# Optimization experiments

Hardware: AMD Instinct MI355X
Metric: run time of the kernel (lower is better)

Reference implementation:

```python
import jax, jax.numpy as jnp
import numpy as np
import math

B, L, DIM = 2, 2048, 1024
NUM_HEADS, QUANTUM_HEADS, CHUNK = 16, 2, 64
HD = DIM // NUM_HEADS  # 64 == CHUNK (required by the original broadcast)
TH = NUM_HEADS - QUANTUM_HEADS
STEPS = 2048
LN_EPS = 1e-5


def setup_inputs() -> dict:
    key = jax.random.key(0)
    ks = jax.random.split(key, 12)
    inp = {
        'x': jax.random.normal(ks[0], (B, L, DIM), dtype=jnp.float32),
        # to_quantum_state: Linear(HD, 2HD) + LayerNorm(2HD) + Tanh
        'wq1': jax.random.normal(ks[1], (HD, 2 * HD), dtype=jnp.float32) * 0.05,
        'bq1': jnp.zeros((2 * HD,), dtype=jnp.float32),
        'ln_g': jnp.ones((2 * HD,), dtype=jnp.float32),
        'ln_b': jnp.zeros((2 * HD,), dtype=jnp.float32),
        'phase_shifts': jax.random.normal(ks[2], (QUANTUM_HEADS,), dtype=jnp.float32) * 0.02,
        'freqs': jax.random.normal(ks[3], (QUANTUM_HEADS,), dtype=jnp.float32) * 0.02,
        # traditional heads: q/k/v projections, no bias
        'wq': jax.random.normal(ks[4], (DIM, TH * HD), dtype=jnp.float32) * 0.02,
        'wk': jax.random.normal(ks[5], (DIM, TH * HD), dtype=jnp.float32) * 0.02,
        'wv': jax.random.normal(ks[6], (DIM, TH * HD), dtype=jnp.float32) * 0.02,
        # output projection
        'wo': jax.random.normal(ks[7], (DIM, DIM), dtype=jnp.float32) * 0.02,
        'bo': jnp.zeros((DIM,), dtype=jnp.float32),
    }
    return inp


def _quantum_state(t, wq1, bq1, ln_g, ln_b):
    # Linear -> LayerNorm -> Tanh; split into (amp, phase)
    h = t @ wq1 + bq1
    mu = h.mean(-1, keepdims=True)
    var = ((h - mu) ** 2).mean(-1, keepdims=True)
    h = (h - mu) * jax.lax.rsqrt(var + LN_EPS) * ln_g + ln_b
    h = jnp.tanh(h)
    return h[..., :HD], h[..., HD:]


def reference(x, wq1, bq1, ln_g, ln_b, phase_shifts, freqs, wq, wk, wv, wo, bo):
    two_pi = 2.0 * math.pi
    angles = jnp.linspace(0.0, two_pi, STEPS)  # torch.linspace is endpoint-inclusive
    cos_table = jnp.cos(angles)
    inv_sqrt_hd = 1.0 / math.sqrt(HD)
    nc = L // CHUNK

    quantum_outs = []
    for h in range(QUANTUM_HEADS):
        xh = x[..., h * HD:(h + 1) * HD]                       # [B,L,HD]
        amp, phase = _quantum_state(xh, wq1, bq1, ln_g, ln_b)  # each [B,L,HD]
        qa = amp.reshape(B, nc, CHUNK, HD)
        qp = phase.reshape(B, nc, CHUNK, HD)
        # keys/values are truncated to the FIRST `chunk` tokens (original quirk)
        ka = amp[:, :CHUNK]        # [B,CHUNK,HD]
        kp = phase[:, :CHUNK]
        v = xh[:, :CHUNK]
        # phase_diff[b,c,i,j] = qp[b,c,i,j] - kp[b,j,i]  (needs CHUNK == HD)
        pd = (qp - jnp.swapaxes(kp, -1, -2)[:, None]) * freqs[h] + phase_shifts[h]
        idx = jnp.mod(pd / two_pi * STEPS, STEPS).astype(jnp.int32)  # in [0, STEPS)
        interference = cos_table[idx]                          # [B,nc,CHUNK,CHUNK]
        scores = jnp.einsum('bcih,bjh->bcij', qa, ka) * interference
        attn = jax.nn.softmax(scores * inv_sqrt_hd, axis=-1)
        out = jnp.einsum('bcij,bjh->bcih', attn, v).reshape(B, L, HD)
        quantum_outs.append(out)

    # traditional multi-head attention on full x
    q = (x @ wq).reshape(B, L, TH, HD)
    k = (x @ wk).reshape(B, L, TH, HD)
    vv = (x @ wv).reshape(B, L, TH, HD)
    scores = jnp.einsum('bqhd,bkhd->bhqk', q, k) * inv_sqrt_hd
    attn = jax.nn.softmax(scores, axis=-1)
    trad = jnp.einsum('bhqk,bkhd->bqhd', attn, vv).reshape(B, L, TH * HD)

    out = jnp.concatenate(quantum_outs + [trad], axis=-1)  # [B,L,DIM]
    return out @ wo + bo
```

## Files before the change

### kernel.cpp

```cpp
#include <hip/hip_runtime.h>
#include <hip/hip_bf16.h>
#include <math.h>

#define B_ 2
#define L_ 2048
#define DIM_ 1024
#define HD_ 64
#define TH_ 14
#define TWO_PI_F 6.28318530717958647692f
#define QSCALE_F 0.1803368801111204f

typedef __bf16 bf16_t;
typedef __bf16 bf16x8 __attribute__((ext_vector_type(8)));
typedef __bf16 bf16x4 __attribute__((ext_vector_type(4)));
typedef float f32x4 __attribute__((ext_vector_type(4)));
typedef float f32x16 __attribute__((ext_vector_type(16)));
typedef unsigned int u32x2 __attribute__((ext_vector_type(2)));

static __device__ __forceinline__ bf16_t f2b(float f) { return (bf16_t)f; }

static __device__ __forceinline__ float fexp2(float x) {
#if __has_builtin(__builtin_amdgcn_exp2f)
  return __builtin_amdgcn_exp2f(x);
#else
  return exp2f(x);
#endif
}

static __device__ __forceinline__ unsigned int cvtpk(float a, float b) {
  unsigned int r;
  asm("v_cvt_pk_bf16_f32 %0, %1, %2" : "=v"(r) : "v"(a), "v"(b));
  return r;
}

static __device__ __forceinline__ void gl16(const bf16_t* g, bf16_t* l) {
  __builtin_amdgcn_global_load_lds(
      (const __attribute__((address_space(1))) void*)g,
      (__attribute__((address_space(3))) void*)l, 16, 0, 0);
}

static __device__ __forceinline__ void swap32(unsigned int& a, unsigned int& b) {
#if __has_builtin(__builtin_amdgcn_permlane32_swap)
  u32x2 r = __builtin_amdgcn_permlane32_swap(a, b, false, false);
  a = r[0];
  b = r[1];
#else
  const int l = (int)(threadIdx.x & 63);
  unsigned int bp_a = (unsigned int)__builtin_amdgcn_ds_bpermute((l ^ 32) << 2, (int)a);
  unsigned int bp_b = (unsigned int)__builtin_amdgcn_ds_bpermute((l ^ 32) << 2, (int)b);
  unsigned int na = (l < 32) ? a : bp_b;
  unsigned int nb = (l < 32) ? bp_a : b;
  a = na;
  b = nb;
#endif
}

__global__ __launch_bounds__(256)
void k_prep(const float* __restrict__ x, const float* __restrict__ wq1,
            const float* __restrict__ bq1, const float* __restrict__ ln_g,
            const float* __restrict__ ln_b, const float* __restrict__ wq,
            const float* __restrict__ wk, const float* __restrict__ wv,
            const float* __restrict__ wo, bf16_t* __restrict__ xb,
            bf16_t* __restrict__ wt_qkv, bf16_t* __restrict__ wt_o,
            bf16_t* __restrict__ amp_b, float* __restrict__ phase) {
  __shared__ float tile[32][33];
  const int t = threadIdx.x;
  const int bid = blockIdx.x;
  if (bid < 4096) {
    const int i = bid * 256 + t;
    const float4 v4 = ((const float4*)x)[i];
    bf16x4 o = {f2b(v4.x), f2b(v4.y), f2b(v4.z), f2b(v4.w)};
    *(bf16x4*)(xb + 4 * (size_t)i) = o;
  } else if (bid < 7808) {
    const float* W;
    bf16_t* Wt;
    int N, kt, nt;
    if (bid < 6784) {
      int r = bid - 4096;
      const int which = r / 896;
      r -= which * 896;
      W = (which == 0) ? wq : (which == 1) ? wk : wv;
      Wt = wt_qkv + (size_t)which * 896 * 1024;
      N = 896;
      kt = r & 31;
      nt = r >> 5;
    } else {
      const int r = bid - 6784;
      W = wo;
      Wt = wt_o;
      N = 1024;
      kt = r & 31;
      nt = r >> 5;
    }
    const int tx = t & 31, ty = t >> 5;
    const int k0 = kt * 32, n0 = nt * 32;
    #pragma unroll
    for (int i = 0; i < 4; ++i)
      tile[ty + 8 * i][tx] = W[(size_t)(k0 + ty + 8 * i) * N + n0 + tx];
    __syncthreads();
    #pragma unroll
    for (int i = 0; i < 4; ++i)
      Wt[(size_t)(n0 + ty + 8 * i) * 1024 + k0 + tx] = f2b(tile[tx][ty + 8 * i]);
  } else {
    const int gw = ((bid - 7808) * 256 + t) >> 6;
    const int lane = t & 63;
    const int h = gw >> 12;
    const int bl = gw & 4095;
    const float xv = x[(size_t)bl * DIM_ + h * HD_ + lane];
    float acc0 = bq1[lane];
    float acc1 = bq1[64 + lane];
    #pragma unroll 16
    for (int kk = 0; kk < 64; ++kk) {
      const float xk = __shfl(xv, kk, 64);
      acc0 = fmaf(xk, wq1[kk * 128 + lane], acc0);
      acc1 = fmaf(xk, wq1[kk * 128 + 64 + lane], acc1);
    }
    float s = acc0 + acc1;
    #pragma unroll
    for (int off = 32; off > 0; off >>= 1) s += __shfl_xor(s, off, 64);
    const float mu = s * (1.0f / 128.0f);
    const float d0 = acc0 - mu, d1 = acc1 - mu;
    float vsum = d0 * d0 + d1 * d1;
    #pragma unroll
    for (int off = 32; off > 0; off >>= 1) vsum += __shfl_xor(vsum, off, 64);
    const float rstd = rsqrtf(vsum * (1.0f / 128.0f) + 1e-5f);
    const float av = tanhf(d0 * rstd * ln_g[lane] + ln_b[lane]);
    const float pv = tanhf(d1 * rstd * ln_g[64 + lane] + ln_b[64 + lane]);
    const size_t o = ((size_t)h * (B_ * L_) + bl) * HD_ + lane;
    amp_b[o] = f2b(av);
    phase[o] = pv;
  }
}

__global__ __launch_bounds__(256)
void k_mm1q(const bf16_t* __restrict__ A, const bf16_t* __restrict__ Wt,
            bf16_t* __restrict__ qb, bf16_t* __restrict__ kb, bf16_t* __restrict__ vb,
            const bf16_t* __restrict__ amp_b, const float* __restrict__ phase,
            const float* __restrict__ shifts, const float* __restrict__ freqs,
            bf16_t* __restrict__ catb) {
  __shared__ char smem[32768];
  const int t = threadIdx.x;
  const int lane = t & 63, w = t >> 6;
  const int bid = blockIdx.x;
  const int v = (bid & 7) * 100 + (bid >> 3);
  if (v < 672) {
    bf16_t* Asm = (bf16_t*)smem;
    bf16_t* Bsm = (bf16_t*)(smem + 16384);
    const int wm = w >> 1, wn = w & 1;
    const int l15 = lane & 15, g = lane >> 4;
    const int m0 = (v & 31) * 128;
    const int n0 = (v >> 5) * 128;
    f32x4 acc[4][4] = {};
    for (int k0 = 0; k0 < 1024; k0 += 64) {
      __syncthreads();
      #pragma unroll
      for (int qc = 0; qc < 4; ++qc) {
        const int idx = t + 256 * qc;
        const int r = idx >> 3, cb = idx & 7;
        const int c = (cb ^ (r & 7)) * 8;
        gl16(A + (size_t)(m0 + r) * 1024 + k0 + c, Asm + w * 512 + qc * 2048);
        gl16(Wt + (size_t)(n0 + r) * 1024 + k0 + c, Bsm + w * 512 + qc * 2048);
      }
      __syncthreads();
      #pragma unroll
      for (int ks = 0; ks < 2; ++ks) {
        bf16x8 af[4], bfr[4];
        #pragma unroll
        for (int mi = 0; mi < 4; ++mi) {
          const int row = wm * 64 + mi * 16 + l15;
          af[mi] = *(const bf16x8*)((char*)Asm + row * 128 + (((ks * 4 + g) ^ (row & 7)) << 4));
        }
        #pragma unroll
        for (int ni = 0; ni < 4; ++ni) {
          const int row = wn * 64 + ni * 16 + l15;
          bfr[ni] = *(const bf16x8*)((char*)Bsm + row * 128 + (((ks * 4 + g) ^ (row & 7)) << 4));
        }
        #pragma unroll
        for (int mi = 0; mi < 4; ++mi)
          #pragma unroll
          for (int ni = 0; ni < 4; ++ni)
            acc[mi][ni] = __builtin_amdgcn_mfma_f32_16x16x32_bf16(bfr[ni], af[mi], acc[mi][ni], 0, 0, 0);
      }
    }
    const int n0w = n0 + wn * 64;
    const int which = (n0 >= 1792) ? 2 : (n0 >= 896) ? 1 : 0;
    #pragma unroll
    for (int mi = 0; mi < 4; ++mi) {
      const int m = m0 + wm * 64 + mi * 16 + (lane & 15);
      const int bsel = m >> 11, ll = m & 2047;
      #pragma unroll
      for (int ni = 0; ni < 4; ++ni) {
        const int nb = n0w + ni * 16 + (lane >> 4) * 4;
        const int nn = nb - which * 896;
        const int head = nn >> 6, hd = nn & 63;
        if (which == 2) {
          #pragma unroll
          for (int r = 0; r < 4; ++r)
            vb[(((size_t)bsel * TH_ + head) * HD_ + hd + r) * L_ + ll] = f2b(acc[mi][ni][r]);
        } else {
          const float sc = (which == 0) ? QSCALE_F : 1.0f;
          bf16_t* dst = (which == 0) ? qb : kb;
          bf16x4 pk;
          #pragma unroll
          for (int r = 0; r < 4; ++r) pk[r] = f2b(acc[mi][ni][r] * sc);
          *(bf16x4*)(dst + (((size_t)bsel * TH_ + head) * L_ + ll) * HD_ + hd) = pk;
        }
      }
    }
  } else {
    bf16_t* Kam = (bf16_t*)smem;
    bf16_t* Vt  = (bf16_t*)(smem + 8192);
    bf16_t* Ps  = (bf16_t*)(smem + 16384);
    const int l15 = lane & 15, g = lane >> 4;
    const int qv = v - 672;
    const int c = qv & 31;
    const int hb = qv >> 5;
    const int b = hb & 1;
    const int h = hb >> 1;
    const size_t abase = ((size_t)h * B_ + b) * L_ * HD_;

    {
      const int r0 = t >> 3, cb0 = t & 7;
      const int r1 = r0 + 32;
      gl16(amp_b + abase + r0 * 64 + (cb0 ^ (r0 & 7)) * 8, Kam + w * 512);
      gl16(amp_b + abase + r1 * 64 + (cb0 ^ (r1 & 7)) * 8, Kam + w * 512 + 2048);
    }
    {
      const int vj = t >> 2;
      const int vd0 = (t & 3) * 16;
      const bf16x8 va = *(const bf16x8*)(A + ((size_t)b * L_ + vj) * DIM_ + h * 64 + vd0);
      const bf16x8 vb2 = *(const bf16x8*)(A + ((size_t)b * L_ + vj) * DIM_ + h * 64 + vd0 + 8);
      #pragma unroll
      for (int e = 0; e < 8; ++e) {
        int d = vd0 + e;
        *(bf16_t*)((char*)Vt + d * 128 + (((vj >> 3) ^ (d & 7)) << 4) + (vj & 7) * 2) = va[e];
        d = vd0 + 8 + e;
        *(bf16_t*)((char*)Vt + d * 128 + (((vj >> 3) ^ (d & 7)) << 4) + (vj & 7) * 2) = vb2[e];
      }
    }
    __syncthreads();

    bf16x8 qf[2];
    {
      const size_t ro = abase + (size_t)(c * 64 + 16 * w + l15) * 64 + g * 8;
      qf[0] = *(const bf16x8*)(amp_b + ro);
      qf[1] = *(const bf16x8*)(amp_b + ro + 32);
    }
    f32x4 s[4] = {};
    #pragma unroll
    for (int ks = 0; ks < 2; ++ks) {
      #pragma unroll
      for (int nt = 0; nt < 4; ++nt) {
        const int jr = nt * 16 + l15;
        const bf16x8 kf = *(const bf16x8*)((char*)Kam + jr * 128 + (((ks * 4 + g) ^ (jr & 7)) << 4));
        s[nt] = __builtin_amdgcn_mfma_f32_16x16x32_bf16(qf[ks], kf, s[nt], 0, 0, 0);
      }
    }
    const float freq = freqs[h], shift = shifts[h];
    char* PsW = (char*)Ps + w * 2048;
    float l_acc[4];
    #pragma unroll
    for (int r = 0; r < 4; ++r) {
      const int i_loc = 16 * w + 4 * g + r;
      const float* qrow = phase + abase + (size_t)(c * 64 + i_loc) * 64;
      const float* krow = phase + abase + i_loc;
      const int row = g * 4 + r;
      float ls = 0.0f;
      #pragma unroll
      for (int nt = 0; nt < 4; ++nt) {
        const int j = nt * 16 + l15;
        const float qp = qrow[j];
        const float kp = krow[j * 64];
        const float pd = (qp - kp) * freq + shift;
        const float t1 = pd * (2048.0f / TWO_PI_F);
        float mm = fmodf(t1, 2048.0f);
        if (mm < 0.0f) mm += 2048.0f;
        int idx = (int)mm;
        idx = idx > 2047 ? 2047 : idx;
        const float interf = cosf((float)idx * (TWO_PI_F / 2047.0f));
        const float sc = s[nt][r] * interf * 0.125f;
        const float e = expf(sc);
        ls += e;
        *(bf16_t*)(PsW + row * 128 + (((j >> 3) ^ (row & 7)) << 4) + (j & 7) * 2) = f2b(e);
      }
      #pragma unroll
      for (int off = 1; off < 16; off <<= 1) ls += __shfl_xor(ls, off, 64);
      l_acc[r] = ls;
    }
    f32x4 o[4] = {};
    #pragma unroll
    for (int ks = 0; ks < 2; ++ks) {
      const bf16x8 pa = *(const bf16x8*)(PsW + l15 * 128 + (((ks * 4 + g) ^ (l15 & 7)) << 4));
      #pragma unroll
      for (int nt = 0; nt < 4; ++nt) {
        const int dr = nt * 16 + l15;
        const bf16x8 vf = *(const bf16x8*)((char*)Vt + dr * 128 + (((ks * 4 + g) ^ (dr & 7)) << 4));
        o[nt] = __builtin_amdgcn_mfma_f32_16x16x32_bf16(pa, vf, o[nt], 0, 0, 0);
      }
    }
    #pragma unroll
    for (int r = 0; r < 4; ++r) {
      const float inv = 1.0f / l_acc[r];
      const int qrow = c * 64 + 16 * w + g * 4 + r;
      #pragma unroll
      for (int nt = 0; nt < 4; ++nt)
        catb[((size_t)b * L_ + qrow) * DIM_ + h * 64 + nt * 16 + l15] = f2b(o[nt][r] * inv);
    }
  }
}

__global__ __launch_bounds__(256)
void k_mm0(const bf16_t* __restrict__ A, const bf16_t* __restrict__ Wt,
           const float* __restrict__ bias, float* __restrict__ outf) {
  __shared__ bf16_t Asm[128 * 64];
  __shared__ bf16_t Bsm[128 * 64];
  const int t = threadIdx.x;
  const int lane = t & 63, w = t >> 6;
  const int wm = w >> 1, wn = w & 1;
  const int l15 = lane & 15, g = lane >> 4;
  const int bid = blockIdx.x;
  const int v = (bid & 7) * 32 + (bid >> 3);
  const int m0 = (v & 31) * 128;
  const int n0 = (v >> 5) * 128;
  f32x4 acc[4][4] = {};
  for (int k0 = 0; k0 < 1024; k0 += 64) {
    __syncthreads();
    #pragma unroll
    for (int qc = 0; qc < 4; ++qc) {
      const int idx = t + 256 * qc;
      const int r = idx >> 3, cb = idx & 7;
      const int c = (cb ^ (r & 7)) * 8;
      gl16(A + (size_t)(m0 + r) * 1024 + k0 + c, Asm + w * 512 + qc * 2048);
      gl16(Wt + (size_t)(n0 + r) * 1024 + k0 + c, Bsm + w * 512 + qc * 2048);
    }
    __syncthreads();
    #pragma unroll
    for (int ks = 0; ks < 2; ++ks) {
      bf16x8 af[4], bfr[4];
      #pragma unroll
      for (int mi = 0; mi < 4; ++mi) {
        const int row = wm * 64 + mi * 16 + l15;
        af[mi] = *(const bf16x8*)((char*)Asm + row * 128 + (((ks * 4 + g) ^ (row & 7)) << 4));
      }
      #pragma unroll
      for (int ni = 0; ni < 4; ++ni) {
        const int row = wn * 64 + ni * 16 + l15;
        bfr[ni] = *(const bf16x8*)((char*)Bsm + row * 128 + (((ks * 4 + g) ^ (row & 7)) << 4));
      }
      #pragma unroll
      for (int mi = 0; mi < 4; ++mi)
        #pragma unroll
        for (int ni = 0; ni < 4; ++ni)
          acc[mi][ni] = __builtin_amdgcn_mfma_f32_16x16x32_bf16(bfr[ni], af[mi], acc[mi][ni], 0, 0, 0);
    }
  }
  #pragma unroll
  for (int mi = 0; mi < 4; ++mi) {
    const int m = m0 + wm * 64 + mi * 16 + l15;
    #pragma unroll
    for (int ni = 0; ni < 4; ++ni) {
      const int nb = n0 + wn * 64 + ni * 16 + g * 4;
      const float4 bv = *(const float4*)&bias[nb];
      float4 r4;
      r4.x = acc[mi][ni][0] + bv.x;
      r4.y = acc[mi][ni][1] + bv.y;
      r4.z = acc[mi][ni][2] + bv.z;
      r4.w = acc[mi][ni][3] + bv.w;
      *(float4*)&outf[(size_t)m * 1024 + nb] = r4;
    }
  }
}

__global__ __launch_bounds__(512)
void k_flash2(const bf16_t* __restrict__ qg, const bf16_t* __restrict__ kg,
              const bf16_t* __restrict__ vt, bf16_t* __restrict__ catb) {
  __shared__ char smem[65536];
  const int t = threadIdx.x;
  const int lane = t & 63, w = t >> 6;
  const int g2 = w >> 2, wl = w & 3;
  const int l31 = lane & 31, hi = lane >> 5;
  int bid = blockIdx.x;
  bid = (bid & 7) * 56 + (bid >> 3);
  const int qblk = bid & 15, bh = bid >> 4;
  const int head = bh % TH_, b = bh / TH_;
  const size_t base = (size_t)bh * (L_ * HD_);
  const int q = qblk * 128 + wl * 32 + l31;
  const int tl = t & 255;
  const int r0 = tl >> 3, cb0 = tl & 7;
  const int r1 = r0 + 32;
  const int c0 = (cb0 ^ (r0 & 7)) * 8;
  const int c1 = (cb0 ^ (r1 & 7)) * 8;
  const int ubase = wl * 512;
  bf16_t* Kg = (bf16_t*)(smem + g2 * 32768);
  bf16_t* Vg = (bf16_t*)(smem + g2 * 32768 + 16384);
  const int kt0 = g2 * 16;

  bf16x8 qf[4];
  #pragma unroll
  for (int slot = 0; slot < 4; ++slot)
    qf[slot] = *(const bf16x8*)(qg + base + (size_t)q * 64 + 16 * slot + 8 * hi);

  f32x16 oT[2] = {};
  float l_acc = 0.0f;

  {
    const bf16_t* ksrc = kg + base + (size_t)kt0 * 64 * 64;
    const bf16_t* vsrc = vt + base + kt0 * 64;
    gl16(ksrc + r0 * 64 + c0, Kg + ubase);
    gl16(ksrc + r1 * 64 + c1, Kg + ubase + 2048);
    gl16(vsrc + (size_t)r0 * L_ + c0, Vg + ubase);
    gl16(vsrc + (size_t)r1 * L_ + c1, Vg + ubase + 2048);
  }
  for (int kt = 0; kt < 16; ++kt) {
    const int cur = kt & 1;
    if (kt < 15) {
      const bf16_t* ksrc = kg + base + (size_t)(kt0 + kt + 1) * 64 * 64;
      const bf16_t* vsrc = vt + base + (kt0 + kt + 1) * 64;
      bf16_t* kd = Kg + (cur ^ 1) * 4096;
      bf16_t* vd = Vg + (cur ^ 1) * 4096;
      gl16(ksrc + r0 * 64 + c0, kd + ubase);
      gl16(ksrc + r1 * 64 + c1, kd + ubase + 2048);
      gl16(vsrc + (size_t)r0 * L_ + c0, vd + ubase);
      gl16(vsrc + (size_t)r1 * L_ + c1, vd + ubase + 2048);
      asm volatile("s_waitcnt vmcnt(4)" ::: "memory");
    } else {
      asm volatile("s_waitcnt vmcnt(0)" ::: "memory");
    }
    __builtin_amdgcn_sched_barrier(0);
    __builtin_amdgcn_s_barrier();
    const char* Kc = (const char*)(Kg + cur * 4096);
    const char* Vc = (const char*)(Vg + cur * 4096);
    f32x16 sT0 = {}, sT1 = {};
    __builtin_amdgcn_s_setprio(1);
    #pragma unroll
    for (int slot = 0; slot < 4; ++slot) {
      const int row0 = l31;
      const int row1 = 32 + l31;
      const bf16x8 kf0 = *(const bf16x8*)(Kc + row0 * 128 + (((2 * slot + hi) ^ (row0 & 7)) << 4));
      const bf16x8 kf1 = *(const bf16x8*)(Kc + row1 * 128 + (((2 * slot + hi) ^ (row1 & 7)) << 4));
      sT0 = __builtin_amdgcn_mfma_f32_32x32x16_bf16(kf0, qf[slot], sT0, 0, 0, 0);
      sT1 = __builtin_amdgcn_mfma_f32_32x32x16_bf16(kf1, qf[slot], sT1, 0, 0, 0);
    }
    __builtin_amdgcn_s_setprio(0);
    unsigned int W0[8], W1[8];
    float la = 0.0f;
    #pragma unroll
    for (int rp = 0; rp < 8; ++rp) {
      const float p00 = fexp2(sT0[2 * rp]);
      const float p01 = fexp2(sT0[2 * rp + 1]);
      const float p10 = fexp2(sT1[2 * rp]);
      const float p11 = fexp2(sT1[2 * rp + 1]);
      la += (p00 + p01) + (p10 + p11);
      W0[rp] = cvtpk(p00, p01);
      W1[rp] = cvtpk(p10, p11);
    }
    l_acc += la;
    unsigned int pb[4][4];
    #pragma unroll
    for (int m1 = 0; m1 < 2; ++m1) {
      unsigned int u, vv;
      u = W0[m1];     vv = W0[2 + m1]; swap32(u, vv); pb[0][m1] = u; pb[0][m1 + 2] = vv;
      u = W0[4 + m1]; vv = W0[6 + m1]; swap32(u, vv); pb[1][m1] = u; pb[1][m1 + 2] = vv;
      u = W1[m1];     vv = W1[2 + m1]; swap32(u, vv); pb[2][m1] = u; pb[2][m1 + 2] = vv;
      u = W1[4 + m1]; vv = W1[6 + m1]; swap32(u, vv); pb[3][m1] = u; pb[3][m1 + 2] = vv;
    }
    __builtin_amdgcn_s_setprio(1);
    #pragma unroll
    for (int slot = 0; slot < 4; ++slot) {
      union { unsigned int u[4]; bf16x8 v8; } pf;
      pf.u[0] = pb[slot][0]; pf.u[1] = pb[slot][1];
      pf.u[2] = pb[slot][2]; pf.u[3] = pb[slot][3];
      #pragma unroll
      for (int dt = 0; dt < 2; ++dt) {
        const int row = 32 * dt + l31;
        const bf16x8 vf = *(const bf16x8*)(Vc + row * 128 + (((2 * slot + hi) ^ (row & 7)) << 4));
        oT[dt] = __builtin_amdgcn_mfma_f32_32x32x16_bf16(vf, pf.v8, oT[dt], 0, 0, 0);
      }
    }
    __builtin_amdgcn_s_setprio(0);
    __builtin_amdgcn_s_barrier();
  }
  const float l_w = l_acc + __shfl_xor(l_acc, 32, 64);
  __syncthreads();
  float* obuf = (float*)(smem + 32768);
  float* lbuf = (float*)smem;
  if (g2 == 1) {
    #pragma unroll
    for (int dt = 0; dt < 2; ++dt)
      #pragma unroll
      for (int e = 0; e < 16; ++e)
        obuf[(dt * 16 + e) * 256 + wl * 64 + lane] = oT[dt][e];
    lbuf[wl * 64 + lane] = l_w;
  }
  __syncthreads();
  if (g2 == 0) {
    const float l_tot = l_w + lbuf[wl * 64 + lane];
    const float inv = 1.0f / l_tot;
    const size_t obase = ((size_t)b * L_ + q) * DIM_ + 128 + head * 64;
    #pragma unroll
    for (int dt = 0; dt < 2; ++dt) {
      #pragma unroll
      for (int rq = 0; rq < 4; ++rq) {
        bf16x4 pk;
        #pragma unroll
        for (int e = 0; e < 4; ++e)
          pk[e] = f2b((oT[dt][4 * rq + e] +
                       obuf[(dt * 16 + 4 * rq + e) * 256 + wl * 64 + lane]) * inv);
        *(bf16x4*)(catb + obase + 32 * dt + 8 * rq + 4 * hi) = pk;
      }
    }
  }
}

extern "C" void kernel_launch(void* const* d_in, const int* in_sizes, int n_in,
                              void* d_out, int out_size, void* d_ws, size_t ws_size,
                              hipStream_t stream) {
  (void)in_sizes; (void)n_in; (void)out_size; (void)ws_size;
  const float* x      = (const float*)d_in[0];
  const float* wq1    = (const float*)d_in[1];
  const float* bq1    = (const float*)d_in[2];
  const float* ln_g   = (const float*)d_in[3];
  const float* ln_b   = (const float*)d_in[4];
  const float* shifts = (const float*)d_in[5];
  const float* freqs  = (const float*)d_in[6];
  const float* wq     = (const float*)d_in[7];
  const float* wk     = (const float*)d_in[8];
  const float* wv     = (const float*)d_in[9];
  const float* wo     = (const float*)d_in[10];
  const float* bo     = (const float*)d_in[11];
  float* out = (float*)d_out;

  char* p = (char*)d_ws;
  bf16_t* amp_b  = (bf16_t*)p; p += (size_t)2 * B_ * L_ * HD_ * 2;
  float* phase   = (float*)p;  p += (size_t)2 * B_ * L_ * HD_ * 4;
  bf16_t* xb     = (bf16_t*)p; p += (size_t)B_ * L_ * DIM_ * 2;
  bf16_t* wt_qkv = (bf16_t*)p; p += (size_t)2688 * 1024 * 2;
  bf16_t* wt_o   = (bf16_t*)p; p += (size_t)1024 * 1024 * 2;
  bf16_t* qb     = (bf16_t*)p; p += (size_t)B_ * TH_ * L_ * HD_ * 2;
  bf16_t* kb     = (bf16_t*)p; p += (size_t)B_ * TH_ * L_ * HD_ * 2;
  bf16_t* vtb    = (bf16_t*)p; p += (size_t)B_ * TH_ * L_ * HD_ * 2;
  bf16_t* catb   = (bf16_t*)p;

  k_prep<<<dim3(9856), dim3(256), 0, stream>>>(x, wq1, bq1, ln_g, ln_b,
                                               wq, wk, wv, wo,
                                               xb, wt_qkv, wt_o, amp_b, phase);
  k_mm1q<<<dim3(800), dim3(256), 0, stream>>>(xb, wt_qkv, qb, kb, vtb,
                                              amp_b, phase, shifts, freqs, catb);
  k_flash2<<<dim3(448), dim3(512), 0, stream>>>(qb, kb, vtb, catb);
  k_mm0<<<dim3(256), dim3(256), 0, stream>>>(catb, wt_o, bo, out);
}
```

Measured before the change: 129.7 us.

## Switch GEMMs to 32x32x16 MFMA and remap mm1q blocks per XCD

Both GEMM kernels (the fused QKV projection and the output projection) now use 32x32x16 bf16 MFMA instructions with 2x2 accumulator tiles per wave instead of 4x4 tiles of 16x16x32. This cuts LDS fragment reads per MFMA and uses the larger MFMA shape. The epilogues are rewritten for the new accumulator lane layout. The mm1q kernel also remaps block IDs so each XCD handles a contiguous group of M rows across all N tiles plus a fixed share of the quantum-head blocks, aiming for better L2 reuse.

```diff
diff --git a/kernel.cpp b/kernel.cpp
--- a/kernel.cpp
+++ b/kernel.cpp
@@ -142,15 +142,17 @@
   const int t = threadIdx.x;
   const int lane = t & 63, w = t >> 6;
   const int bid = blockIdx.x;
-  const int v = (bid & 7) * 100 + (bid >> 3);
-  if (v < 672) {
+  const int xcd = bid & 7, slot = bid >> 3;
+  if (slot < 84) {
     bf16_t* Asm = (bf16_t*)smem;
     bf16_t* Bsm = (bf16_t*)(smem + 16384);
     const int wm = w >> 1, wn = w & 1;
-    const int l15 = lane & 15, g = lane >> 4;
-    const int m0 = (v & 31) * 128;
-    const int n0 = (v >> 5) * 128;
-    f32x4 acc[4][4] = {};
+    const int l31 = lane & 31, hi = lane >> 5;
+    const int m_blk = xcd * 4 + slot / 21;
+    const int n_blk = slot % 21;
+    const int m0 = m_blk * 128;
+    const int n0 = n_blk * 128;
+    f32x16 acc[2][2] = {};
     for (int k0 = 0; k0 < 1024; k0 += 64) {
       __syncthreads();
       #pragma unroll
@@ -163,47 +165,50 @@
       }
       __syncthreads();
       #pragma unroll
-      for (int ks = 0; ks < 2; ++ks) {
-        bf16x8 af[4], bfr[4];
-        #pragma unroll
-        for (int mi = 0; mi < 4; ++mi) {
-          const int row = wm * 64 + mi * 16 + l15;
-          af[mi] = *(const bf16x8*)((char*)Asm + row * 128 + (((ks * 4 + g) ^ (row & 7)) << 4));
-        }
-        #pragma unroll
-        for (int ni = 0; ni < 4; ++ni) {
-          const int row = wn * 64 + ni * 16 + l15;
-          bfr[ni] = *(const bf16x8*)((char*)Bsm + row * 128 + (((ks * 4 + g) ^ (row & 7)) << 4));
-        }
-        #pragma unroll
-        for (int mi = 0; mi < 4; ++mi)
-          #pragma unroll
-          for (int ni = 0; ni < 4; ++ni)
-            acc[mi][ni] = __builtin_amdgcn_mfma_f32_16x16x32_bf16(bfr[ni], af[mi], acc[mi][ni], 0, 0, 0);
+      for (int s = 0; s < 4; ++s) {
+        const int ra0 = wm * 64 + l31, ra1 = ra0 + 32;
+        const int rb0 = wn * 64 + l31, rb1 = rb0 + 32;
+        const bf16x8 af0 = *(const bf16x8*)((char*)Asm + ra0 * 128 + (((2 * s + hi) ^ (ra0 & 7)) << 4));
+        const bf16x8 af1 = *(const bf16x8*)((char*)Asm + ra1 * 128 + (((2 * s + hi) ^ (ra1 & 7)) << 4));
+        const bf16x8 bf0 = *(const bf16x8*)((char*)Bsm + rb0 * 128 + (((2 * s + hi) ^ (rb0 & 7)) << 4));
+        const bf16x8 bf1 = *(const bf16x8*)((char*)Bsm + rb1 * 128 + (((2 * s + hi) ^ (rb1 & 7)) << 4));
+        acc[0][0] = __builtin_amdgcn_mfma_f32_32x32x16_bf16(bf0, af0, acc[0][0], 0, 0, 0);
+        acc[0][1] = __builtin_amdgcn_mfma_f32_32x32x16_bf16(bf1, af0, acc[0][1], 0, 0, 0);
+        acc[1][0] = __builtin_amdgcn_mfma_f32_32x32x16_bf16(bf0, af1, acc[1][0], 0, 0, 0);
+        acc[1][1] = __builtin_amdgcn_mfma_f32_32x32x16_bf16(bf1, af1, acc[1][1], 0, 0, 0);
       }
     }
     const int n0w = n0 + wn * 64;
     const int which = (n0 >= 1792) ? 2 : (n0 >= 896) ? 1 : 0;
     #pragma unroll
-    for (int mi = 0; mi < 4; ++mi) {
-      const int m = m0 + wm * 64 + mi * 16 + (lane & 15);
+    for (int mi = 0; mi < 2; ++mi) {
+      const int m = m0 + wm * 64 + mi * 32 + l31;
       const int bsel = m >> 11, ll = m & 2047;
       #pragma unroll
-      for (int ni = 0; ni < 4; ++ni) {
-        const int nb = n0w + ni * 16 + (lane >> 4) * 4;
-        const int nn = nb - which * 896;
-        const int head = nn >> 6, hd = nn & 63;
+      for (int ni = 0; ni < 2; ++ni) {
         if (which == 2) {
           #pragma unroll
-          for (int r = 0; r < 4; ++r)
-            vb[(((size_t)bsel * TH_ + head) * HD_ + hd + r) * L_ + ll] = f2b(acc[mi][ni][r]);
+          for (int rp = 0; rp < 4; ++rp) {
+            #pragma unroll
+            for (int e = 0; e < 4; ++e) {
+              const int nn = n0w + ni * 32 + 8 * rp + 4 * hi + e - 1792;
+              const int head = nn >> 6, hd = nn & 63;
+              vb[(((size_t)bsel * TH_ + head) * HD_ + hd) * L_ + ll] = f2b(acc[mi][ni][4 * rp + e]);
+            }
+          }
         } else {
           const float sc = (which == 0) ? QSCALE_F : 1.0f;
           bf16_t* dst = (which == 0) ? qb : kb;
-          bf16x4 pk;
           #pragma unroll
-          for (int r = 0; r < 4; ++r) pk[r] = f2b(acc[mi][ni][r] * sc);
-          *(bf16x4*)(dst + (((size_t)bsel * TH_ + head) * L_ + ll) * HD_ + hd) = pk;
+          for (int rp = 0; rp < 4; ++rp) {
+            const int nb = n0w + ni * 32 + 8 * rp + 4 * hi;
+            const int nn = nb - which * 896;
+            const int head = nn >> 6, hd = nn & 63;
+            bf16x4 pk;
+            #pragma unroll
+            for (int e = 0; e < 4; ++e) pk[e] = f2b(acc[mi][ni][4 * rp + e] * sc);
+            *(bf16x4*)(dst + (((size_t)bsel * TH_ + head) * L_ + ll) * HD_ + hd) = pk;
+          }
         }
       }
     }
@@ -212,7 +217,7 @@
     bf16_t* Vt  = (bf16_t*)(smem + 8192);
     bf16_t* Ps  = (bf16_t*)(smem + 16384);
     const int l15 = lane & 15, g = lane >> 4;
-    const int qv = v - 672;
+    const int qv = xcd * 16 + (slot - 84);
     const int c = qv & 31;
     const int hb = qv >> 5;
     const int b = hb & 1;
@@ -317,12 +322,12 @@
   const int t = threadIdx.x;
   const int lane = t & 63, w = t >> 6;
   const int wm = w >> 1, wn = w & 1;
-  const int l15 = lane & 15, g = lane >> 4;
+  const int l31 = lane & 31, hi = lane >> 5;
   const int bid = blockIdx.x;
   const int v = (bid & 7) * 32 + (bid >> 3);
   const int m0 = (v & 31) * 128;
   const int n0 = (v >> 5) * 128;
-  f32x4 acc[4][4] = {};
+  f32x16 acc[2][2] = {};
   for (int k0 = 0; k0 < 1024; k0 += 64) {
     __syncthreads();
     #pragma unroll
@@ -335,38 +340,35 @@
     }
     __syncthreads();
     #pragma unroll
-    for (int ks = 0; ks < 2; ++ks) {
-      bf16x8 af[4], bfr[4];
-      #pragma unroll
-      for (int mi = 0; mi < 4; ++mi) {
-        const int row = wm * 64 + mi * 16 + l15;
-        af[mi] = *(const bf16x8*)((char*)Asm + row * 128 + (((ks * 4 + g) ^ (row & 7)) << 4));
-      }
-      #pragma unroll
-      for (int ni = 0; ni < 4; ++ni) {
-        const int row = wn * 64 + ni * 16 + l15;
-        bfr[ni] = *(const bf16x8*)((char*)Bsm + row * 128 + (((ks * 4 + g) ^ (row & 7)) << 4));
-      }
-      #pragma unroll
-      for (int mi = 0; mi < 4; ++mi)
-        #pragma unroll
-        for (int ni = 0; ni < 4; ++ni)
-          acc[mi][ni] = __builtin_amdgcn_mfma_f32_16x16x32_bf16(bfr[ni], af[mi], acc[mi][ni], 0, 0, 0);
+    for (int s = 0; s < 4; ++s) {
+      const int ra0 = wm * 64 + l31, ra1 = ra0 + 32;
+      const int rb0 = wn * 64 + l31, rb1 = rb0 + 32;
+      const bf16x8 af0 = *(const bf16x8*)((char*)Asm + ra0 * 128 + (((2 * s + hi) ^ (ra0 & 7)) << 4));
+      const bf16x8 af1 = *(const bf16x8*)((char*)Asm + ra1 * 128 + (((2 * s + hi) ^ (ra1 & 7)) << 4));
+      const bf16x8 bf0 = *(const bf16x8*)((char*)Bsm + rb0 * 128 + (((2 * s + hi) ^ (rb0 & 7)) << 4));
+      const bf16x8 bf1 = *(const bf16x8*)((char*)Bsm + rb1 * 128 + (((2 * s + hi) ^ (rb1 & 7)) << 4));
+      acc[0][0] = __builtin_amdgcn_mfma_f32_32x32x16_bf16(bf0, af0, acc[0][0], 0, 0, 0);
+      acc[0][1] = __builtin_amdgcn_mfma_f32_32x32x16_bf16(bf1, af0, acc[0][1], 0, 0, 0);
+      acc[1][0] = __builtin_amdgcn_mfma_f32_32x32x16_bf16(bf0, af1, acc[1][0], 0, 0, 0);
+      acc[1][1] = __builtin_amdgcn_mfma_f32_32x32x16_bf16(bf1, af1, acc[1][1], 0, 0, 0);
     }
   }
   #pragma unroll
-  for (int mi = 0; mi < 4; ++mi) {
-    const int m = m0 + wm * 64 + mi * 16 + l15;
-    #pragma unroll
-    for (int ni = 0; ni < 4; ++ni) {
-      const int nb = n0 + wn * 64 + ni * 16 + g * 4;
-      const float4 bv = *(const float4*)&bias[nb];
-      float4 r4;
-      r4.x = acc[mi][ni][0] + bv.x;
-      r4.y = acc[mi][ni][1] + bv.y;
-      r4.z = acc[mi][ni][2] + bv.z;
-      r4.w = acc[mi][ni][3] + bv.w;
-      *(float4*)&outf[(size_t)m * 1024 + nb] = r4;
+  for (int mi = 0; mi < 2; ++mi) {
+    const int m = m0 + wm * 64 + mi * 32 + l31;
+    #pragma unroll
+    for (int ni = 0; ni < 2; ++ni) {
+      #pragma unroll
+      for (int rp = 0; rp < 4; ++rp) {
+        const int nb = n0 + wn * 64 + ni * 32 + 8 * rp + 4 * hi;
+        const float4 bv = *(const float4*)&bias[nb];
+        float4 r4;
+        r4.x = acc[mi][ni][4 * rp + 0] + bv.x;
+        r4.y = acc[mi][ni][4 * rp + 1] + bv.y;
+        r4.z = acc[mi][ni][4 * rp + 2] + bv.z;
+        r4.w = acc[mi][ni][4 * rp + 3] + bv.w;
+        *(float4*)&outf[(size_t)m * 1024 + nb] = r4;
+      }
     }
   }
 }
```

Measured after the change: 121.0 us. -6.7%, faster.
